# Kernel tuning notes

Measured on AMD Instinct MI355X. Metric: run time of the kernel, lower is better.

## Reference

```python
import jax, jax.numpy as jnp
import numpy as np

B, S, E = 2, 2048, 1024
H = 16
DH = E // H
FF = 4096
LN_EPS = 1e-5


def setup_inputs() -> dict:
    key = jax.random.key(0)
    ks = jax.random.split(key, 8)
    s_in = 1.0 / np.sqrt(E)
    s_ff = 1.0 / np.sqrt(FF)
    return {
        "x": jax.random.normal(ks[0], (B, S, E), dtype=jnp.float32),
        "w_qkv": jax.random.normal(ks[1], (E, 3 * E), dtype=jnp.float32) * s_in,
        "b_qkv": jnp.zeros((3 * E,), dtype=jnp.float32),
        "w_proj": jax.random.normal(ks[2], (E, E), dtype=jnp.float32) * s_in,
        "b_proj": jnp.zeros((E,), dtype=jnp.float32),
        "ln_g": jnp.ones((E,), dtype=jnp.float32),
        "ln_b": jnp.zeros((E,), dtype=jnp.float32),
        "w1": jax.random.normal(ks[3], (E, FF), dtype=jnp.float32) * s_in,
        "b1": jnp.zeros((FF,), dtype=jnp.float32),
        "w2": jax.random.normal(ks[4], (FF, E), dtype=jnp.float32) * s_ff,
        "b2": jnp.zeros((E,), dtype=jnp.float32),
    }


def reference(x, w_qkv, b_qkv, w_proj, b_proj, ln_g, ln_b, w1, b1, w2, b2):
    b, s, e = x.shape
    scale = e ** 0.5  # NOTE: original scales by sqrt(embed_dim), not sqrt(head_dim)
    # qkv projection then raw view to [B,3,H,S,Dh] (faithful to torch .view)
    qkv = (x @ w_qkv + b_qkv).reshape(b, 3, H, s, DH)
    q, k, v = qkv[:, 0], qkv[:, 1], qkv[:, 2]  # each [B,H,S,Dh]
    scores = jnp.einsum("bhqd,bhkd->bhqk", q, k) / scale  # [B,H,S,S]
    causal = jnp.tril(jnp.ones((s, s), dtype=bool))
    scores = jnp.where(causal, scores, -jnp.inf)
    attn = jax.nn.softmax(scores, axis=-1)
    h = jnp.einsum("bhqk,bhkd->bhqd", attn, v)  # [B,H,S,Dh]
    h = h.reshape(b, s, e)  # faithful raw view back to [B,S,E]
    h = h @ w_proj + b_proj  # dropout = identity (eval)
    # add & norm
    h = h + x
    mu = jnp.mean(h, axis=-1, keepdims=True)
    var = jnp.var(h, axis=-1, keepdims=True)
    h = (h - mu) * jax.lax.rsqrt(var + LN_EPS) * ln_g + ln_b
    # FFN (dropouts = identity in eval)
    out = jax.nn.relu(h @ w1 + b1) @ w2 + b2
    return out
```

## Files before the change

### kernel.cpp

```cpp
#include <hip/hip_runtime.h>

#define B_ 2
#define S_ 2048
#define E_ 1024
#define H_ 16
#define DH_ 64
#define FF_ 4096

typedef unsigned short bf16_t;
typedef __attribute__((ext_vector_type(8))) short bfrag;
typedef __attribute__((ext_vector_type(4))) float f32x4;
typedef __attribute__((ext_vector_type(16))) float f32x16;
typedef __attribute__((ext_vector_type(4))) unsigned int u32x4;

__device__ __forceinline__ bf16_t f2bf(float x) {
  union { float f; unsigned u; } c; c.f = x;
  return (bf16_t)((c.u + 0x7fffu + ((c.u >> 16) & 1u)) >> 16);
}

__device__ __forceinline__ unsigned pkbf(float lo, float hi) {
  unsigned r;
  asm("v_cvt_pk_bf16_f32 %0, %1, %2" : "=v"(r) : "v"(lo), "v"(hi));
  return r;
}

__device__ __forceinline__ void gload16(const void* g, void* l) {
  __builtin_amdgcn_global_load_lds(
      (const __attribute__((address_space(1))) void*)g,
      (__attribute__((address_space(3))) void*)l, 16, 0, 0);
}

__global__ __launch_bounds__(256) void cvt_kernel(const float* __restrict__ s,
                                                  bf16_t* __restrict__ d) {
  const int i = blockIdx.x * 256 + threadIdx.x;
  const float4 v = ((const float4*)s)[i];
  union { bf16_t u[4]; uint2 uv; } o;
  o.u[0] = f2bf(v.x); o.u[1] = f2bf(v.y); o.u[2] = f2bf(v.z); o.u[3] = f2bf(v.w);
  *(uint2*)(d + (size_t)i * 4) = o.uv;
}

__global__ void transpose_cvt(const float* __restrict__ src, bf16_t* __restrict__ dst,
                              int R, int C) {
  __shared__ float tile[32][33];
  const int c0 = blockIdx.x * 32, r0 = blockIdx.y * 32;
  const int tx = threadIdx.x, ty = threadIdx.y;
#pragma unroll
  for (int i = 0; i < 32; i += 8)
    tile[ty + i][tx] = src[(size_t)(r0 + ty + i) * C + c0 + tx];
  __syncthreads();
#pragma unroll
  for (int i = 0; i < 32; i += 8)
    dst[(size_t)(c0 + ty + i) * R + r0 + tx] = f2bf(tile[tx][ty + i]);
}

__global__ void vtrans_kernel(const bf16_t* __restrict__ qkv, bf16_t* __restrict__ vt) {
  const int bh = blockIdx.z;
  const int b = bh >> 4, h = bh & 15;
  const bf16_t* src = qkv + (size_t)b * S_ * 3 * E_ + (size_t)2 * H_ * S_ * DH_ +
                      (size_t)h * S_ * DH_;
  bf16_t* dst = vt + (size_t)bh * DH_ * S_;
  const int s0 = blockIdx.x * 32, d0 = blockIdx.y * 32;
  __shared__ bf16_t tile[32][33];
  const int tx = threadIdx.x, ty = threadIdx.y;
#pragma unroll
  for (int i = 0; i < 32; i += 8)
    tile[ty + i][tx] = src[(size_t)(s0 + ty + i) * DH_ + d0 + tx];
  __syncthreads();
#pragma unroll
  for (int i = 0; i < 32; i += 8)
    dst[(size_t)(d0 + ty + i) * S_ + s0 + tx] = tile[tx][ty + i];
}


__device__ __forceinline__ void stage_half(const bf16_t* __restrict__ G, int row0,
                                           int kbyte, int Kbytes, bf16_t* ldsreg,
                                           int w, int l) {
#pragma unroll
  for (int j = 0; j < 2; ++j) {
    const int chunk = j * 8 + w;
    const int r = chunk * 8 + (l >> 3);
    const int slot = ((l & 7) ^ (r & 7)) << 4;
    const char* src = (const char*)G + (size_t)(row0 + r) * Kbytes + kbyte + slot;
    gload16(src, (char*)ldsreg + chunk * 1024);
  }
}

__device__ __forceinline__ bfrag ldfrag(const bf16_t* __restrict__ reg, int r, int ks,
                                        int l) {
  int cb = ks * 64 + ((l >> 4) << 4);
  cb ^= (r & 7) << 4;
  return *(const bfrag*)((const char*)reg + r * 128 + cb);
}

template <int MODE>
__global__ __launch_bounds__(512, 2) void gemm8(
    const bf16_t* __restrict__ A, const bf16_t* __restrict__ Bt,
    const float* __restrict__ bias, const float* __restrict__ resid,
    float* __restrict__ outF, bf16_t* __restrict__ outB,
    int M, int N, int K, int ktiles) {
  __shared__ __align__(16) bf16_t lds4[4][256 * 64];
  const int tid = threadIdx.x;
  const int w = tid >> 6, l = tid & 63;
  const int wr = (w >> 2) * 128, wc = (w & 3) * 64;
  const int m0t = blockIdx.y * 256, n0t = blockIdx.x * 256;
  const int Kb = K * 2;
  const int kt0 = (MODE == 4) ? (int)blockIdx.z * ktiles : 0;
  const int ktEnd = kt0 + ktiles;
  if (MODE == 4) outF += (size_t)blockIdx.z * (size_t)M * N;

  stage_half(A, m0t, kt0 * 128, Kb, lds4[0], w, l);
  stage_half(A, m0t + 128, kt0 * 128, Kb, lds4[0] + 8192, w, l);
  stage_half(Bt, n0t, kt0 * 128, Kb, lds4[1], w, l);
  stage_half(Bt, n0t + 128, kt0 * 128, Kb, lds4[1] + 8192, w, l);
  stage_half(Bt, n0t, (kt0 + 1) * 128, Kb, lds4[3], w, l);
  stage_half(Bt, n0t + 128, (kt0 + 1) * 128, Kb, lds4[3] + 8192, w, l);
  asm volatile("s_waitcnt vmcnt(4)" ::: "memory");
  __builtin_amdgcn_s_barrier();

  f32x4 acc[8][4] = {};
  const int fr = l & 15;

  for (int t2 = kt0; t2 < ktEnd; t2 += 2) {
#pragma unroll
    for (int d = 0; d < 2; ++d) {
      const bf16_t* Ar = lds4[d * 2];
      const bf16_t* Br = lds4[d * 2 + 1];
      int sa = t2 + 1 + d; if (sa >= ktEnd) sa = kt0;
      int sb = t2 + 2 + d; if (sb >= ktEnd) sb = kt0;
      bfrag bfr[4][2], afr[2][2];
#pragma unroll
      for (int p = 0; p < 4; ++p) {
        if (p == 0) {
#pragma unroll
          for (int n = 0; n < 4; ++n)
#pragma unroll
            for (int ks = 0; ks < 2; ++ks)
              bfr[n][ks] = ldfrag(Br, wc + n * 16 + fr, ks, l);
        }
#pragma unroll
        for (int mm = 0; mm < 2; ++mm)
#pragma unroll
          for (int ks = 0; ks < 2; ++ks)
            afr[mm][ks] = ldfrag(Ar, wr + p * 32 + mm * 16 + fr, ks, l);
        if (p == 0)      stage_half(A, m0t, sa * 128, Kb, lds4[(d ^ 1) * 2], w, l);
        else if (p == 1) stage_half(A, m0t + 128, sa * 128, Kb, lds4[(d ^ 1) * 2] + 8192, w, l);
        else if (p == 2) stage_half(Bt, n0t, sb * 128, Kb, lds4[d * 2 + 1], w, l);
        else             stage_half(Bt, n0t + 128, sb * 128, Kb, lds4[d * 2 + 1] + 8192, w, l);
        __builtin_amdgcn_s_barrier();
        asm volatile("s_waitcnt lgkmcnt(0)" ::: "memory");
        __builtin_amdgcn_sched_barrier(0);
        __builtin_amdgcn_s_setprio(1);
#pragma unroll
        for (int mm = 0; mm < 2; ++mm)
#pragma unroll
          for (int n = 0; n < 4; ++n)
#pragma unroll
            for (int ks = 0; ks < 2; ++ks)
              acc[p * 2 + mm][n] = __builtin_amdgcn_mfma_f32_16x16x32_bf16(
                  afr[mm][ks], bfr[n][ks], acc[p * 2 + mm][n], 0, 0, 0);
        __builtin_amdgcn_s_setprio(0);
        if (p == 3) asm volatile("s_waitcnt vmcnt(4)" ::: "memory");
        __builtin_amdgcn_s_barrier();
      }
    }
  }

  const int cr = (l >> 4) * 4, cc = l & 15;
#pragma unroll
  for (int n = 0; n < 4; ++n) {
    const int gc = n0t + wc + n * 16 + cc;
    const float bn = (MODE == 4) ? 0.f : bias[gc];
#pragma unroll
    for (int m = 0; m < 8; ++m) {
      const int gr0 = m0t + wr + m * 16 + cr;
#pragma unroll
      for (int j = 0; j < 4; ++j) {
        float v = acc[m][n][j] + bn;
        const size_t idx = (size_t)(gr0 + j) * N + gc;
        if (MODE == 1) v += resid[idx];
        if (MODE == 2) v = fmaxf(v, 0.f);
        if (MODE == 0 || MODE == 2) outB[idx] = f2bf(v);
        else outF[idx] = v;
      }
    }
  }
}

__global__ __launch_bounds__(256) void red2_kernel(const float* __restrict__ p,
                                                   const float* __restrict__ bias,
                                                   float* __restrict__ out) {
  const size_t i = ((size_t)blockIdx.x * 256 + threadIdx.x) * 4;
  const size_t PS = (size_t)4096 * 1024;
  const float4 a = *(const float4*)(p + i);
  const float4 b = *(const float4*)(p + PS + i);
  const float4 bb = *(const float4*)(bias + (i & 1023));
  float4 o;
  o.x = a.x + b.x + bb.x;
  o.y = a.y + b.y + bb.y;
  o.z = a.z + b.z + bb.z;
  o.w = a.w + b.w + bb.w;
  *(float4*)(out + i) = o;
}

#define C1_ 0.0450842213f

struct kf4 { bfrag k[4]; };

__device__ __forceinline__ kf4 loadK32(const bf16_t* __restrict__ Kp, int kv0,
                                       int lq32, int hi) {
  kf4 r;
#pragma unroll
  for (int c = 0; c < 4; ++c)
    r.k[c] = *(const bfrag*)&Kp[(size_t)(kv0 + lq32) * DH_ + c * 16 + hi * 8];
  return r;
}

template <bool MASK>
__device__ __forceinline__ void compute32(const kf4& s, const bf16_t* __restrict__ Vt,
                                          int kv0, const bfrag* qf, f32x16& o0,
                                          f32x16& o1, float& m, float& lsum,
                                          int lq32, int hi) {
  bfrag v00, v01, v10, v11;
  {
    const bf16_t* vr = &Vt[(size_t)lq32 * S_ + kv0 + hi * 8];
    v00 = *(const bfrag*)vr;
    v01 = *(const bfrag*)(vr + 16);
    const bf16_t* vr2 = &Vt[(size_t)(32 + lq32) * S_ + kv0 + hi * 8];
    v10 = *(const bfrag*)vr2;
    v11 = *(const bfrag*)(vr2 + 16);
  }
  f32x16 st;
#pragma unroll
  for (int j = 0; j < 16; ++j) st[j] = 0.f;
#pragma unroll
  for (int c = 0; c < 4; ++c)
    st = __builtin_amdgcn_mfma_f32_32x32x16_bf16(s.k[c], qf[c], st, 0, 0, 0);
  if (MASK) {
#pragma unroll
    for (int r = 0; r < 16; ++r) {
      const int kvloc = (r & 3) + 8 * (r >> 2) + 4 * hi;
      st[r] = (kvloc <= lq32) ? st[r] : -3.0e38f;
    }
  }
  float mx[8];
#pragma unroll
  for (int j = 0; j < 8; ++j) mx[j] = fmaxf(st[j], st[j + 8]);
#pragma unroll
  for (int stp = 4; stp >= 1; stp >>= 1)
#pragma unroll
    for (int j = 0; j < stp; ++j) mx[j] = fmaxf(mx[j], mx[j + stp]);
  float pm = fmaxf(mx[0], __shfl_xor(mx[0], 32));
  if (!__all(pm <= m + 128.0f)) {
    const float mn = fmaxf(m, pm);
    const float corr = exp2f((m - mn) * C1_);
    m = mn;
    lsum *= corr;
#pragma unroll
    for (int j = 0; j < 16; ++j) { o0[j] *= corr; o1[j] *= corr; }
  }
  const float mc = m * C1_;
  float p[16];
#pragma unroll
  for (int j = 0; j < 16; ++j) p[j] = exp2f(__builtin_fmaf(st[j], C1_, -mc));
  float sm[8];
#pragma unroll
  for (int j = 0; j < 8; ++j) sm[j] = p[j] + p[j + 8];
#pragma unroll
  for (int stp = 4; stp >= 1; stp >>= 1)
#pragma unroll
    for (int j = 0; j < stp; ++j) sm[j] += sm[j + stp];
  lsum += sm[0] + __shfl_xor(sm[0], 32);
  unsigned wv[8], ov[8];
#pragma unroll
  for (int j = 0; j < 8; ++j) wv[j] = pkbf(p[2 * j], p[2 * j + 1]);
#pragma unroll
  for (int j = 0; j < 8; ++j) ov[j] = (unsigned)__shfl_xor((int)wv[j], 32);
  union { unsigned u[4]; bfrag f; } f0, f1;
  f0.u[0] = hi ? ov[2] : wv[0];  f0.u[1] = hi ? ov[3] : wv[1];
  f0.u[2] = hi ? wv[2] : ov[0];  f0.u[3] = hi ? wv[3] : ov[1];
  f1.u[0] = hi ? ov[6] : wv[4];  f1.u[1] = hi ? ov[7] : wv[5];
  f1.u[2] = hi ? wv[6] : ov[4];  f1.u[3] = hi ? wv[7] : ov[5];
  o0 = __builtin_amdgcn_mfma_f32_32x32x16_bf16(v00, f0.f, o0, 0, 0, 0);
  o1 = __builtin_amdgcn_mfma_f32_32x32x16_bf16(v10, f0.f, o1, 0, 0, 0);
  o0 = __builtin_amdgcn_mfma_f32_32x32x16_bf16(v01, f1.f, o0, 0, 0, 0);
  o1 = __builtin_amdgcn_mfma_f32_32x32x16_bf16(v11, f1.f, o1, 0, 0, 0);
}

__global__ __launch_bounds__(256, 2) void attn_kernel(const bf16_t* __restrict__ qkv,
                                                      const bf16_t* __restrict__ vt,
                                                      bf16_t* __restrict__ outp) {
  __shared__ unsigned short otl[4][32 * 72];
  const int tid = threadIdx.x;
  const int w = tid >> 6, l = tid & 63;
  const int lq32 = l & 31, hi = l >> 5;
  const int lid = blockIdx.x;
  const int xcd = lid & 7;
  const int i = lid >> 3;
  const int by = xcd * 4 + (i & 3);
  const int qi = i >> 2;
  const int qt = (qi & 1) ? (15 - (qi >> 1)) : (qi >> 1);
  const int b = by >> 4, h = by & 15;
  const size_t bbase = (size_t)b * S_ * 3 * E_;
  const bf16_t* Q = qkv + bbase + (size_t)h * S_ * DH_;
  const bf16_t* Kp = Q + (size_t)H_ * S_ * DH_;
  const bf16_t* Vt = vt + (size_t)by * DH_ * S_;
  bf16_t* Og = outp + (size_t)by * S_ * DH_;
  const int q0w = qt * 128 + w * 32;

  bfrag qf[4];
#pragma unroll
  for (int c = 0; c < 4; ++c)
    qf[c] = *(const bfrag*)&Q[(size_t)(q0w + lq32) * DH_ + c * 16 + hi * 8];

  f32x16 o0, o1;
#pragma unroll
  for (int j = 0; j < 16; ++j) { o0[j] = 0.f; o1[j] = 0.f; }
  float m = -3.0e38f, lsum = 0.f;

  const int nsteps = q0w >> 5;
  kf4 kcur = loadK32(Kp, 0, lq32, hi);
  for (int s = 0; s < nsteps; ++s) {
    kf4 knxt = loadK32(Kp, (s + 1) * 32, lq32, hi);
    compute32<false>(kcur, Vt, s * 32, qf, o0, o1, m, lsum, lq32, hi);
    kcur = knxt;
  }
  compute32<true>(kcur, Vt, q0w, qf, o0, o1, m, lsum, lq32, hi);

  const float linv = 1.0f / lsum;
  unsigned short* otw = otl[w];
#pragma unroll
  for (int t = 0; t < 2; ++t) {
    const f32x16& oo = t ? o1 : o0;
#pragma unroll
    for (int g = 0; g < 4; ++g) {
      const int d = t * 32 + g * 8 + hi * 4;
      uint2 v;
      v.x = pkbf(oo[g * 4 + 0] * linv, oo[g * 4 + 1] * linv);
      v.y = pkbf(oo[g * 4 + 2] * linv, oo[g * 4 + 3] * linv);
      *(uint2*)&otw[lq32 * 72 + d] = v;
    }
  }
  asm volatile("s_waitcnt lgkmcnt(0)" ::: "memory");
  const int q = l >> 1, hh = l & 1;
#pragma unroll
  for (int ii = 0; ii < 4; ++ii) {
    u32x4 v = *(const u32x4*)&otw[q * 72 + hh * 32 + ii * 8];
    *(u32x4*)&Og[(size_t)(q0w + q) * DH_ + hh * 32 + ii * 8] = v;
  }
}

__device__ __forceinline__ void ln_core(float4 v, int t, const float* g,
                                        const float* be, bf16_t* orow) {
  float s = v.x + v.y + v.z + v.w;
  float q = v.x * v.x + v.y * v.y + v.z * v.z + v.w * v.w;
#pragma unroll
  for (int d = 1; d < 64; d <<= 1) { s += __shfl_xor(s, d); q += __shfl_xor(q, d); }
  __shared__ float red[8];
  const int w = t >> 6;
  if ((t & 63) == 0) { red[w] = s; red[4 + w] = q; }
  __syncthreads();
  s = red[0] + red[1] + red[2] + red[3];
  q = red[4] + red[5] + red[6] + red[7];
  const float mu = s * (1.f / E_);
  const float var = q * (1.f / E_) - mu * mu;
  const float rs = rsqrtf(var + 1e-5f);
  const float4 gg = ((const float4*)g)[t];
  const float4 bb = ((const float4*)be)[t];
  union { bf16_t u[4]; uint2 uv; } o;
  o.u[0] = f2bf((v.x - mu) * rs * gg.x + bb.x);
  o.u[1] = f2bf((v.y - mu) * rs * gg.y + bb.y);
  o.u[2] = f2bf((v.z - mu) * rs * gg.z + bb.z);
  o.u[3] = f2bf((v.w - mu) * rs * gg.w + bb.w);
  *(uint2*)(orow + t * 4) = o.uv;
}

__global__ __launch_bounds__(256) void ln_kernel(const float* __restrict__ hin,
                                                 const float* __restrict__ g,
                                                 const float* __restrict__ be,
                                                 bf16_t* __restrict__ outp) {
  const int row = blockIdx.x, t = threadIdx.x;
  const float4 v = ((const float4*)(hin + (size_t)row * E_))[t];
  ln_core(v, t, g, be, outp + (size_t)row * E_);
}

__global__ __launch_bounds__(256) void ln2_kernel(const float* __restrict__ p,
                                                  const float* __restrict__ x,
                                                  const float* __restrict__ bproj,
                                                  const float* __restrict__ g,
                                                  const float* __restrict__ be,
                                                  bf16_t* __restrict__ outp) {
  const int row = blockIdx.x, t = threadIdx.x;
  const size_t PS = (size_t)4096 * 1024;
  const size_t off = (size_t)row * E_ + t * 4;
  const float4 a = *(const float4*)(p + off);
  const float4 b = *(const float4*)(p + PS + off);
  const float4 xr = *(const float4*)(x + off);
  const float4 bp = *(const float4*)(bproj + t * 4);
  float4 v;
  v.x = a.x + b.x + xr.x + bp.x;
  v.y = a.y + b.y + xr.y + bp.y;
  v.z = a.z + b.z + xr.z + bp.z;
  v.w = a.w + b.w + xr.w + bp.w;
  ln_core(v, t, g, be, outp + (size_t)row * E_);
}

extern "C" void kernel_launch(void* const* d_in, const int* in_sizes, int n_in,
                              void* d_out, int out_size, void* d_ws, size_t ws_size,
                              hipStream_t stream) {
  (void)in_sizes; (void)n_in; (void)out_size;
  const float* x      = (const float*)d_in[0];
  const float* w_qkv  = (const float*)d_in[1];
  const float* b_qkv  = (const float*)d_in[2];
  const float* w_proj = (const float*)d_in[3];
  const float* b_proj = (const float*)d_in[4];
  const float* ln_g   = (const float*)d_in[5];
  const float* ln_b   = (const float*)d_in[6];
  const float* w1     = (const float*)d_in[7];
  const float* b1     = (const float*)d_in[8];
  const float* w2     = (const float*)d_in[9];
  const float* b2     = (const float*)d_in[10];
  float* out = (float*)d_out;
  char* ws = (char*)d_ws;
  const size_t MB = (size_t)1 << 20;
  bf16_t* w2T    = (bf16_t*)(ws + 0 * MB);
  bf16_t* w1T    = (bf16_t*)(ws + 8 * MB);
  bf16_t* vtb    = (bf16_t*)(ws + 16 * MB);
  bf16_t* lnb    = (bf16_t*)(ws + 16 * MB);
  bf16_t* wqkvT  = (bf16_t*)(ws + 24 * MB);
  bf16_t* wprojT = (bf16_t*)(ws + 30 * MB);
  bf16_t* attnb  = (bf16_t*)(ws + 32 * MB);
  bf16_t* xb     = (bf16_t*)(ws + 40 * MB);
  bf16_t* qkvb   = (bf16_t*)(ws + 48 * MB);
  float*  pparts = (float*)(ws + 48 * MB);
  float*  hbuf   = (float*)(ws + 48 * MB);
  bf16_t* ffn1b  = (bf16_t*)(ws + 48 * MB);
  float*  fparts = (float*)(ws + 80 * MB);
  const bool splitk = ws_size >= 112 * MB;

  dim3 tb(32, 8);
  cvt_kernel<<<4096, 256, 0, stream>>>(x, xb);
  transpose_cvt<<<dim3(3072 / 32, 1024 / 32), tb, 0, stream>>>(w_qkv, wqkvT, 1024, 3072);
  transpose_cvt<<<dim3(1024 / 32, 1024 / 32), tb, 0, stream>>>(w_proj, wprojT, 1024, 1024);
  transpose_cvt<<<dim3(4096 / 32, 1024 / 32), tb, 0, stream>>>(w1, w1T, 1024, 4096);
  transpose_cvt<<<dim3(1024 / 32, 4096 / 32), tb, 0, stream>>>(w2, w2T, 4096, 1024);

  gemm8<0><<<dim3(12, 16), 512, 0, stream>>>(xb, wqkvT, b_qkv, nullptr, nullptr, qkvb,
                                             4096, 3072, 1024, 16);

  vtrans_kernel<<<dim3(S_ / 32, 2, 32), tb, 0, stream>>>(qkvb, vtb);
  attn_kernel<<<dim3(512), 256, 0, stream>>>(qkvb, vtb, attnb);

  if (splitk) {
    gemm8<4><<<dim3(4, 16, 2), 512, 0, stream>>>(attnb, wprojT, nullptr, nullptr,
                                                 pparts, nullptr, 4096, 1024, 1024, 8);
    ln2_kernel<<<4096, 256, 0, stream>>>(pparts, x, b_proj, ln_g, ln_b, lnb);
    gemm8<2><<<dim3(16, 16), 512, 0, stream>>>(lnb, w1T, b1, nullptr, nullptr, ffn1b,
                                               4096, 4096, 1024, 16);
    gemm8<4><<<dim3(4, 16, 2), 512, 0, stream>>>(ffn1b, w2T, nullptr, nullptr, fparts,
                                                 nullptr, 4096, 1024, 4096, 32);
    red2_kernel<<<4096, 256, 0, stream>>>(fparts, b2, out);
  } else {
    gemm8<1><<<dim3(4, 16), 512, 0, stream>>>(attnb, wprojT, b_proj, x, hbuf, nullptr,
                                              4096, 1024, 1024, 16);
    ln_kernel<<<4096, 256, 0, stream>>>(hbuf, ln_g, ln_b, lnb);
    gemm8<2><<<dim3(16, 16), 512, 0, stream>>>(lnb, w1T, b1, nullptr, nullptr, ffn1b,
                                               4096, 4096, 1024, 16);
    gemm8<3><<<dim3(4, 16), 512, 0, stream>>>(ffn1b, w2T, b2, nullptr, out, nullptr,
                                              4096, 1024, 4096, 64);
  }
}
```

Before: 292.3 us.

## Use 4-way split-K for projection and FFN2, simplify attention grid

The projection and second FFN GEMMs now split K four ways instead of two, giving 256 blocks each, with reductions widened to sum four partial buffers. Workspace is remapped so the FFN1 output and the FFN2 partials do not overlap. Attention switches to a 2D grid without XCD-aware block remapping and raises the launch-bounds occupancy hint to 3. The extra split-K partials double the reduction traffic, and dropping the XCD mapping may reduce L2 locality for K/V.

```diff
diff --git a/kernel.cpp b/kernel.cpp
--- a/kernel.cpp
+++ b/kernel.cpp
@@ -186,19 +186,21 @@
   }
 }
 
-__global__ __launch_bounds__(256) void red2_kernel(const float* __restrict__ p,
+__global__ __launch_bounds__(256) void red4_kernel(const float* __restrict__ p,
                                                    const float* __restrict__ bias,
                                                    float* __restrict__ out) {
   const size_t i = ((size_t)blockIdx.x * 256 + threadIdx.x) * 4;
   const size_t PS = (size_t)4096 * 1024;
   const float4 a = *(const float4*)(p + i);
   const float4 b = *(const float4*)(p + PS + i);
+  const float4 c = *(const float4*)(p + 2 * PS + i);
+  const float4 d = *(const float4*)(p + 3 * PS + i);
   const float4 bb = *(const float4*)(bias + (i & 1023));
   float4 o;
-  o.x = a.x + b.x + bb.x;
-  o.y = a.y + b.y + bb.y;
-  o.z = a.z + b.z + bb.z;
-  o.w = a.w + b.w + bb.w;
+  o.x = a.x + b.x + c.x + d.x + bb.x;
+  o.y = a.y + b.y + c.y + d.y + bb.y;
+  o.z = a.z + b.z + c.z + d.z + bb.z;
+  o.w = a.w + b.w + c.w + d.w + bb.w;
   *(float4*)(out + i) = o;
 }
 
@@ -286,20 +288,16 @@
   o1 = __builtin_amdgcn_mfma_f32_32x32x16_bf16(v11, f1.f, o1, 0, 0, 0);
 }
 
-__global__ __launch_bounds__(256, 2) void attn_kernel(const bf16_t* __restrict__ qkv,
+__global__ __launch_bounds__(256, 3) void attn_kernel(const bf16_t* __restrict__ qkv,
                                                       const bf16_t* __restrict__ vt,
                                                       bf16_t* __restrict__ outp) {
-  __shared__ unsigned short otl[4][32 * 72];
+  __shared__ unsigned short ot[4][32 * 72];
   const int tid = threadIdx.x;
   const int w = tid >> 6, l = tid & 63;
   const int lq32 = l & 31, hi = l >> 5;
-  const int lid = blockIdx.x;
-  const int xcd = lid & 7;
-  const int i = lid >> 3;
-  const int by = xcd * 4 + (i & 3);
-  const int qi = i >> 2;
-  const int qt = (qi & 1) ? (15 - (qi >> 1)) : (qi >> 1);
+  const int by = blockIdx.y;
   const int b = by >> 4, h = by & 15;
+  const int qt = (by & 16) ? (15 - (int)blockIdx.x) : (int)blockIdx.x;
   const size_t bbase = (size_t)b * S_ * 3 * E_;
   const bf16_t* Q = qkv + bbase + (size_t)h * S_ * DH_;
   const bf16_t* Kp = Q + (size_t)H_ * S_ * DH_;
@@ -327,7 +325,7 @@
   compute32<true>(kcur, Vt, q0w, qf, o0, o1, m, lsum, lq32, hi);
 
   const float linv = 1.0f / lsum;
-  unsigned short* otw = otl[w];
+  unsigned short* otw = ot[w];
 #pragma unroll
   for (int t = 0; t < 2; ++t) {
     const f32x16& oo = t ? o1 : o0;
@@ -343,9 +341,9 @@
   asm volatile("s_waitcnt lgkmcnt(0)" ::: "memory");
   const int q = l >> 1, hh = l & 1;
 #pragma unroll
-  for (int ii = 0; ii < 4; ++ii) {
-    u32x4 v = *(const u32x4*)&otw[q * 72 + hh * 32 + ii * 8];
-    *(u32x4*)&Og[(size_t)(q0w + q) * DH_ + hh * 32 + ii * 8] = v;
+  for (int i = 0; i < 4; ++i) {
+    u32x4 v = *(const u32x4*)&otw[q * 72 + hh * 32 + i * 8];
+    *(u32x4*)&Og[(size_t)(q0w + q) * DH_ + hh * 32 + i * 8] = v;
   }
 }
 
@@ -383,7 +381,7 @@
   ln_core(v, t, g, be, outp + (size_t)row * E_);
 }
 
-__global__ __launch_bounds__(256) void ln2_kernel(const float* __restrict__ p,
+__global__ __launch_bounds__(256) void ln4_kernel(const float* __restrict__ p,
                                                   const float* __restrict__ x,
                                                   const float* __restrict__ bproj,
                                                   const float* __restrict__ g,
@@ -394,13 +392,15 @@
   const size_t off = (size_t)row * E_ + t * 4;
   const float4 a = *(const float4*)(p + off);
   const float4 b = *(const float4*)(p + PS + off);
+  const float4 c = *(const float4*)(p + 2 * PS + off);
+  const float4 d = *(const float4*)(p + 3 * PS + off);
   const float4 xr = *(const float4*)(x + off);
   const float4 bp = *(const float4*)(bproj + t * 4);
   float4 v;
-  v.x = a.x + b.x + xr.x + bp.x;
-  v.y = a.y + b.y + xr.y + bp.y;
-  v.z = a.z + b.z + xr.z + bp.z;
-  v.w = a.w + b.w + xr.w + bp.w;
+  v.x = a.x + b.x + c.x + d.x + xr.x + bp.x;
+  v.y = a.y + b.y + c.y + d.y + xr.y + bp.y;
+  v.z = a.z + b.z + c.z + d.z + xr.z + bp.z;
+  v.w = a.w + b.w + c.w + d.w + xr.w + bp.w;
   ln_core(v, t, g, be, outp + (size_t)row * E_);
 }
 
@@ -432,9 +432,10 @@
   bf16_t* xb     = (bf16_t*)(ws + 40 * MB);
   bf16_t* qkvb   = (bf16_t*)(ws + 48 * MB);
   float*  pparts = (float*)(ws + 48 * MB);
+  bf16_t* ffn1s  = (bf16_t*)(ws + 80 * MB);
+  float*  fparts = (float*)(ws + 16 * MB);
   float*  hbuf   = (float*)(ws + 48 * MB);
-  bf16_t* ffn1b  = (bf16_t*)(ws + 48 * MB);
-  float*  fparts = (float*)(ws + 80 * MB);
+  bf16_t* ffn1f  = (bf16_t*)(ws + 48 * MB);
   const bool splitk = ws_size >= 112 * MB;
 
   dim3 tb(32, 8);
@@ -448,24 +449,24 @@
                                              4096, 3072, 1024, 16);
 
   vtrans_kernel<<<dim3(S_ / 32, 2, 32), tb, 0, stream>>>(qkvb, vtb);
-  attn_kernel<<<dim3(512), 256, 0, stream>>>(qkvb, vtb, attnb);
+  attn_kernel<<<dim3(16, 32), 256, 0, stream>>>(qkvb, vtb, attnb);
 
   if (splitk) {
-    gemm8<4><<<dim3(4, 16, 2), 512, 0, stream>>>(attnb, wprojT, nullptr, nullptr,
-                                                 pparts, nullptr, 4096, 1024, 1024, 8);
-    ln2_kernel<<<4096, 256, 0, stream>>>(pparts, x, b_proj, ln_g, ln_b, lnb);
-    gemm8<2><<<dim3(16, 16), 512, 0, stream>>>(lnb, w1T, b1, nullptr, nullptr, ffn1b,
+    gemm8<4><<<dim3(4, 16, 4), 512, 0, stream>>>(attnb, wprojT, nullptr, nullptr,
+                                                 pparts, nullptr, 4096, 1024, 1024, 4);
+    ln4_kernel<<<4096, 256, 0, stream>>>(pparts, x, b_proj, ln_g, ln_b, lnb);
+    gemm8<2><<<dim3(16, 16), 512, 0, stream>>>(lnb, w1T, b1, nullptr, nullptr, ffn1s,
                                                4096, 4096, 1024, 16);
-    gemm8<4><<<dim3(4, 16, 2), 512, 0, stream>>>(ffn1b, w2T, nullptr, nullptr, fparts,
-                                                 nullptr, 4096, 1024, 4096, 32);
-    red2_kernel<<<4096, 256, 0, stream>>>(fparts, b2, out);
+    gemm8<4><<<dim3(4, 16, 4), 512, 0, stream>>>(ffn1s, w2T, nullptr, nullptr, fparts,
+                                                 nullptr, 4096, 1024, 4096, 16);
+    red4_kernel<<<4096, 256, 0, stream>>>(fparts, b2, out);
   } else {
     gemm8<1><<<dim3(4, 16), 512, 0, stream>>>(attnb, wprojT, b_proj, x, hbuf, nullptr,
                                               4096, 1024, 1024, 16);
     ln_kernel<<<4096, 256, 0, stream>>>(hbuf, ln_g, ln_b, lnb);
-    gemm8<2><<<dim3(16, 16), 512, 0, stream>>>(lnb, w1T, b1, nullptr, nullptr, ffn1b,
+    gemm8<2><<<dim3(16, 16), 512, 0, stream>>>(lnb, w1T, b1, nullptr, nullptr, ffn1f,
                                                4096, 4096, 1024, 16);
-    gemm8<3><<<dim3(4, 16), 512, 0, stream>>>(ffn1b, w2T, b2, nullptr, out, nullptr,
+    gemm8<3><<<dim3(4, 16), 512, 0, stream>>>(ffn1f, w2T, b2, nullptr, out, nullptr,
                                               4096, 1024, 4096, 64);
   }
 }
```

Result: faster. 248.7 us (-14.9%).
